# Optimization experiments

Measured on AMD Instinct MI355X. Metric: run time of the kernel, lower is better.

## Reference

```python
import jax, jax.numpy as jnp
import numpy as np

NUM_GROUPS = 32
EPS = 1e-6


def group_norm(x, gamma, beta):
    # x: [B, C, H, W]
    B, C, H, W = x.shape
    xg = x.reshape(B, NUM_GROUPS, C // NUM_GROUPS, H, W)
    mean = jnp.mean(xg, axis=(2, 3, 4), keepdims=True)
    var = jnp.var(xg, axis=(2, 3, 4), keepdims=True)
    xn = (xg - mean) * jax.lax.rsqrt(var + EPS)
    xn = xn.reshape(B, C, H, W)
    return xn * gamma[None, :, None, None] + beta[None, :, None, None]


def conv1x1(x, w, b):
    # x: [B, C, H, W], w: [Cout, Cin], b: [Cout]
    return jnp.einsum('bchw,dc->bdhw', x, w) + b[None, :, None, None]


def setup_inputs() -> dict:
    key = jax.random.key(0)
    ks = jax.random.split(key, 11)
    B, C, H, W = 4, 512, 64, 64
    s = 1.0 / np.sqrt(C)
    return {
        'x': jax.random.normal(ks[0], (B, C, H, W), dtype=jnp.float32),
        'gn_gamma': jnp.ones((C,), dtype=jnp.float32),
        'gn_beta': jnp.zeros((C,), dtype=jnp.float32),
        'wq': jax.random.normal(ks[1], (C, C), dtype=jnp.float32) * s,
        'bq': jax.random.normal(ks[2], (C,), dtype=jnp.float32) * 0.01,
        'wk': jax.random.normal(ks[3], (C, C), dtype=jnp.float32) * s,
        'bk': jax.random.normal(ks[4], (C,), dtype=jnp.float32) * 0.01,
        'wv': jax.random.normal(ks[5], (C, C), dtype=jnp.float32) * s,
        'bv': jax.random.normal(ks[6], (C,), dtype=jnp.float32) * 0.01,
        'wo': jax.random.normal(ks[7], (C, C), dtype=jnp.float32) * s,
        'bo': jax.random.normal(ks[8], (C,), dtype=jnp.float32) * 0.01,
    }


def reference(x, gn_gamma, gn_beta, wq, bq, wk, bk, wv, bv, wo, bo):
    B, C, H, W = x.shape
    h = group_norm(x, gn_gamma, gn_beta)
    q = conv1x1(h, wq, bq).reshape(B, C, H * W)  # [B, C, N]
    k = conv1x1(h, wk, bk).reshape(B, C, H * W)
    v = conv1x1(h, wv, bv).reshape(B, C, H * W)
    scale = jnp.asarray(C, x.dtype) ** -0.5
    # scores[b, i, j] = q_i . k_j
    scores = jnp.einsum('bci,bcj->bij', q, k) * scale  # [B, N, N]
    attn = jax.nn.softmax(scores, axis=2)
    # out[b, c, i] = sum_j v[b, c, j] * attn[b, i, j]
    out = jnp.einsum('bcj,bij->bci', v, attn).reshape(B, C, H, W)
    out = conv1x1(out, wo, bo)
    return x + out
```

## Files before the change

kernel.cpp:

```cpp
#include <hip/hip_runtime.h>

using uint = unsigned int;
typedef short bf16x8 __attribute__((ext_vector_type(8)));
typedef _Float16 f16x8 __attribute__((ext_vector_type(8)));
typedef float f32x4 __attribute__((ext_vector_type(4)));
typedef long i64;
typedef i64 i64x2 __attribute__((ext_vector_type(2)));

static constexpr int Cc = 512;
static constexpr int Nn = 4096;
static constexpr size_t NC = (size_t)Nn * Cc;
static constexpr size_t SN = (size_t)Nn * Nn;

__device__ __forceinline__ unsigned short f2bf(float f) {
    unsigned int u = __builtin_bit_cast(unsigned int, f);
    u = (u + 0x7fff + ((u >> 16) & 1)) >> 16;
    return (unsigned short)u;
}
__device__ __forceinline__ unsigned short f2h(float f) {
    _Float16 h = (_Float16)f;
    return __builtin_bit_cast(unsigned short, h);
}
__device__ __forceinline__ int perm64(int k) {
    return (k & ~63) | ((k & 0x18) << 1) | ((k & 0x20) >> 2) | (k & 7);
}

__device__ __forceinline__ void gll16(const void* g, void* l) {
    __builtin_amdgcn_global_load_lds(
        (const __attribute__((address_space(1))) void*)g,
        (__attribute__((address_space(3))) void*)l, 16, 0, 0);
}

__global__ void cvt_kernel(const float* __restrict__ in, unsigned short* __restrict__ out, int n4) {
    int i = blockIdx.x * blockDim.x + threadIdx.x;
    if (i < n4) {
        float4 v = ((const float4*)in)[i];
        out[i * 4 + 0] = f2bf(v.x);
        out[i * 4 + 1] = f2bf(v.y);
        out[i * 4 + 2] = f2bf(v.z);
        out[i * 4 + 3] = f2bf(v.w);
    }
}

__global__ void zero_kernel(float* __restrict__ p, int n4) {
    int i = blockIdx.x * blockDim.x + threadIdx.x;
    if (i < n4) ((float4*)p)[i] = make_float4(0.f, 0.f, 0.f, 0.f);
}

__global__ void gn_stats_kernel(const float* __restrict__ x, float* __restrict__ meanb,
                                float* __restrict__ rsb) {
    int bg = blockIdx.x;
    const float* slab = x + (size_t)bg * 16 * Nn;
    const float4* s4 = (const float4*)slab;
    int t = threadIdx.x;
    float s1 = 0.f, s2 = 0.f;
#pragma unroll 8
    for (int k = 0; k < 64; ++k) {
        float4 v = s4[k * 256 + t];
        s1 += v.x + v.y + v.z + v.w;
        s2 += v.x * v.x + v.y * v.y + v.z * v.z + v.w * v.w;
    }
#pragma unroll
    for (int o = 32; o > 0; o >>= 1) { s1 += __shfl_down(s1, o); s2 += __shfl_down(s2, o); }
    __shared__ float r1[4], r2[4];
    int wv_ = t >> 6, ln = t & 63;
    if (ln == 0) { r1[wv_] = s1; r2[wv_] = s2; }
    __syncthreads();
    if (t == 0) {
        float a1 = r1[0] + r1[1] + r1[2] + r1[3];
        float a2 = r2[0] + r2[1] + r2[2] + r2[3];
        float mean = a1 * (1.f / 65536.f);
        float var = a2 * (1.f / 65536.f) - mean * mean;
        meanb[bg] = mean;
        rsb[bg] = rsqrtf(var + 1e-6f);
    }
}

__global__ __launch_bounds__(256) void gn_norm_kernel(
    const float* __restrict__ x, const float* __restrict__ meanb, const float* __restrict__ rsb,
    const float* __restrict__ gamma, const float* __restrict__ beta,
    unsigned short* __restrict__ h_t) {
    __shared__ float tile[64][65];
    int n0 = blockIdx.x * 64, c0 = blockIdx.y * 64, b = blockIdx.z;
    int t = threadIdx.x;
    const float* xb = x + (size_t)b * Cc * Nn;
#pragma unroll
    for (int j = 0; j < 4; ++j) {
        int i = j * 256 + t;
        int c = i >> 4;
        int n4 = i & 15;
        int cg = c0 + c;
        float4 v = ((const float4*)(xb + (size_t)cg * Nn + n0))[n4];
        int g = cg >> 4;
        float mean = meanb[b * 32 + g], rs = rsb[b * 32 + g];
        float ga = gamma[cg] * rs;
        float be = beta[cg] - mean * ga;
        tile[n4 * 4 + 0][c] = v.x * ga + be;
        tile[n4 * 4 + 1][c] = v.y * ga + be;
        tile[n4 * 4 + 2][c] = v.z * ga + be;
        tile[n4 * 4 + 3][c] = v.w * ga + be;
    }
    __syncthreads();
    int n = t >> 2;
    int cpart = (t & 3) * 16;
    unsigned short o[16];
#pragma unroll
    for (int q = 0; q < 16; ++q) o[q] = f2bf(tile[n][cpart + q]);
    unsigned short* dst = h_t + (size_t)b * NC + (size_t)(n0 + n) * Cc + c0 + cpart;
    ((uint4*)dst)[0] = ((uint4*)o)[0];
    ((uint4*)dst)[1] = ((uint4*)o)[1];
}

template <int BM, int DT, int BIAS_MODE, int OUT_MODE, int HAS_RES>
__global__ __launch_bounds__(256, 2) void gemm_bt(
    const unsigned short* __restrict__ A, int lda, size_t sA,
    const unsigned short* __restrict__ Bt, int ldb, size_t sB,
    void* __restrict__ outp, int ldc, size_t sC,
    const float* __restrict__ bias,
    const float* __restrict__ res, size_t sR,
    int K, float alpha) {
    constexpr int MT = BM / 32;
    __shared__ unsigned short lA[2][BM * 64];
    __shared__ unsigned short lB[2][128 * 64];
    int z = blockIdx.z;
    A += (size_t)z * sA;
    Bt += (size_t)z * sB;
    int m0 = blockIdx.y * BM, n0 = blockIdx.x * 128;
    int t = threadIdx.x;
    int lane = t & 63, wave = t >> 6;
    int wm = wave >> 1, wn = wave & 1;
    int lo = lane & 15, quad = lane >> 4;

    f32x4 acc[MT][4];
#pragma unroll
    for (int a1 = 0; a1 < MT; ++a1)
#pragma unroll
        for (int a2 = 0; a2 < 4; ++a2) acc[a1][a2] = (f32x4){0.f, 0.f, 0.f, 0.f};

    auto stage = [&](int buf, int k0) {
#pragma unroll
        for (int p = 0; p < MT; ++p) {
            int ci = p * 256 + t;
            int row = ci >> 3;
            int gs = (ci ^ row) & 7;
            gll16(A + (size_t)(m0 + row) * lda + k0 + gs * 8, &lA[buf][ci * 8]);
        }
#pragma unroll
        for (int p = 0; p < 4; ++p) {
            int ci = p * 256 + t;
            int row = ci >> 3;
            int gs = (ci ^ row) & 7;
            gll16(Bt + (size_t)(n0 + row) * ldb + k0 + gs * 8, &lB[buf][ci * 8]);
        }
    };

    int nk = K >> 6;
    stage(0, 0);
    __syncthreads();
    int cur = 0;
    for (int it = 0; it < nk; ++it) {
        if (it + 1 < nk) stage(cur ^ 1, (it + 1) << 6);
#pragma unroll
        for (int ks = 0; ks < 2; ++ks) {
            int G = quad + ks * 4;
            bf16x8 af[MT], bfr[4];
#pragma unroll
            for (int mt = 0; mt < MT; ++mt) {
                int R = wm * (BM / 2) + mt * 16 + lo;
                af[mt] = *(const bf16x8*)&lA[cur][R * 64 + (((G ^ R) & 7) << 3)];
            }
#pragma unroll
            for (int nt = 0; nt < 4; ++nt) {
                int R = wn * 64 + nt * 16 + lo;
                bfr[nt] = *(const bf16x8*)&lB[cur][R * 64 + (((G ^ R) & 7) << 3)];
            }
#pragma unroll
            for (int mt = 0; mt < MT; ++mt)
#pragma unroll
                for (int nt = 0; nt < 4; ++nt) {
                    if (DT == 0)
                        acc[mt][nt] = __builtin_amdgcn_mfma_f32_16x16x32_bf16(af[mt], bfr[nt], acc[mt][nt], 0, 0, 0);
                    else
                        acc[mt][nt] = __builtin_amdgcn_mfma_f32_16x16x32_f16(
                            __builtin_bit_cast(f16x8, af[mt]), __builtin_bit_cast(f16x8, bfr[nt]),
                            acc[mt][nt], 0, 0, 0);
                }
        }
        __syncthreads();
        cur ^= 1;
    }

    size_t zc = (size_t)z * sC;
    float* outf = (float*)outp + zc;
    unsigned short* outb = (unsigned short*)outp + zc;
    unsigned char* outc = (unsigned char*)outp + zc;
    const float* resz = HAS_RES ? res + (size_t)z * sR : nullptr;

#pragma unroll
    for (int mt = 0; mt < MT; ++mt) {
#pragma unroll
        for (int nt = 0; nt < 4; ++nt) {
            int row = m0 + wm * (BM / 2) + mt * 16 + quad * 4;
            int col = n0 + wn * 64 + nt * 16 + lo;
            float bn = (BIAS_MODE == 2) ? bias[col] : 0.f;
#pragma unroll
            for (int r = 0; r < 4; ++r) {
                float vv = acc[mt][nt][r];
                if (BIAS_MODE == 1) vv += bias[row + r];
                if (BIAS_MODE == 2) vv += bn;
                vv *= alpha;
                if (OUT_MODE == 3) {
                    float e = fmaxf(fminf(vv, 448.f), -448.f);
                    int pk = __builtin_amdgcn_cvt_pk_fp8_f32(e, e, 0, false);
                    outc[(size_t)(row + r) * ldc + perm64(col)] = (unsigned char)(pk & 0xff);
                } else {
                    size_t off = (size_t)(row + r) * ldc + col;
                    if (HAS_RES) vv += resz[off];
                    if (OUT_MODE == 0) outf[off] = vv;
                    else if (OUT_MODE == 1) outb[off] = f2bf(vv);
                    else outb[off] = f2h(vv);
                }
            }
        }
    }
}


__global__ __launch_bounds__(256, 2) void qk_fp8(
    const unsigned char* __restrict__ Q, const unsigned char* __restrict__ Kt,
    unsigned char* __restrict__ S, float* __restrict__ lsum, float alpha) {
    __shared__ unsigned char lA[3][256 * 64];
    __shared__ unsigned char lB[3][128 * 64];
    int z = blockIdx.z;
    Q += (size_t)z * NC;
    Kt += (size_t)z * NC;
    S += (size_t)z * SN;
    lsum += (size_t)z * Nn;
    int m0 = blockIdx.y * 256, n0 = blockIdx.x * 128;
    int t = threadIdx.x;
    int lane = t & 63, wave = t >> 6;
    int wm = wave >> 1, wn = wave & 1;
    int lo = lane & 15, quad = lane >> 4;

    f32x4 acc[8][4];
#pragma unroll
    for (int a1 = 0; a1 < 8; ++a1)
#pragma unroll
        for (int a2 = 0; a2 < 4; ++a2) acc[a1][a2] = (f32x4){0.f, 0.f, 0.f, 0.f};

    auto stage = [&](int buf, int it) {
        int k0 = it * 64;
#pragma unroll
        for (int p = 0; p < 4; ++p) {
            int ci = p * 256 + t;
            int line = ci >> 3;
            int slot = (ci & 7) ^ (line & 7);
            int row = (line << 1) | (slot >> 2);
            int g = slot & 3;
            gll16(Q + (size_t)(m0 + row) * Cc + k0 + g * 16, &lA[buf][ci * 16]);
        }
#pragma unroll
        for (int p = 0; p < 2; ++p) {
            int ci = p * 256 + t;
            int line = ci >> 3;
            int slot = (ci & 7) ^ (line & 7);
            int row = (line << 1) | (slot >> 2);
            int g = slot & 3;
            gll16(Kt + (size_t)(n0 + row) * Cc + k0 + g * 16, &lB[buf][ci * 16]);
        }
    };

    stage(0, 0);
    __builtin_amdgcn_sched_barrier(0);
    stage(1, 1);
    __builtin_amdgcn_sched_barrier(0);
    for (int it = 0; it < 8; ++it) {
        asm volatile("s_waitcnt vmcnt(6)" ::: "memory");
        __builtin_amdgcn_s_barrier();
        asm volatile("" ::: "memory");
        __builtin_amdgcn_sched_barrier(0);
        if (it + 2 < 8) stage((it + 2) % 3, it + 2);
        __builtin_amdgcn_sched_barrier(0);
        int cur = it % 3;
        i64x2 aq[8], bq[4];
#pragma unroll
        for (int mt = 0; mt < 8; ++mt) {
            int R = wm * 128 + mt * 16 + lo;
            int line = R >> 1;
            int slot = (((R & 1) << 2) | quad) ^ (line & 7);
            aq[mt] = *(const i64x2*)&lA[cur][line * 128 + slot * 16];
        }
#pragma unroll
        for (int nt = 0; nt < 4; ++nt) {
            int R = wn * 64 + nt * 16 + lo;
            int line = R >> 1;
            int slot = (((R & 1) << 2) | quad) ^ (line & 7);
            bq[nt] = *(const i64x2*)&lB[cur][line * 128 + slot * 16];
        }
#pragma unroll
        for (int ks = 0; ks < 2; ++ks)
#pragma unroll
            for (int mt = 0; mt < 8; ++mt)
#pragma unroll
                for (int nt = 0; nt < 4; ++nt)
                    acc[mt][nt] = __builtin_amdgcn_mfma_f32_16x16x32_fp8_fp8(
                        aq[mt][ks], bq[nt][ks], acc[mt][nt], 0, 0, 0);
    }

#pragma unroll
    for (int mt = 0; mt < 8; ++mt) {
        int row = m0 + wm * 128 + mt * 16 + quad * 4;
        float rsum[4] = {0.f, 0.f, 0.f, 0.f};
#pragma unroll
        for (int nt = 0; nt < 4; ++nt) {
            int col = n0 + wn * 64 + nt * 16 + lo;
            int colp = perm64(col);
#pragma unroll
            for (int r = 0; r < 4; ++r) {
                float e = __expf(acc[mt][nt][r] * alpha - 2.f);
                e = fminf(e, 448.f);
                int pk = __builtin_amdgcn_cvt_pk_fp8_f32(e, e, 0, false);
                S[(size_t)(row + r) * Nn + colp] = (unsigned char)(pk & 0xff);
                rsum[r] += __builtin_amdgcn_cvt_f32_fp8(pk, 0);
            }
        }
#pragma unroll
        for (int o = 1; o < 16; o <<= 1) {
#pragma unroll
            for (int r = 0; r < 4; ++r) rsum[r] += __shfl_xor(rsum[r], o);
        }
        if (lo == 0) {
#pragma unroll
            for (int r = 0; r < 4; ++r) atomicAdd(&lsum[row + r], rsum[r]);
        }
    }
}

__global__ __launch_bounds__(256, 3) void pv_fp8(
    const unsigned char* __restrict__ S, const unsigned char* __restrict__ V,
    const float* __restrict__ lsum, unsigned short* __restrict__ o_t) {
    __shared__ unsigned char lA[3][128 * 64];
    __shared__ unsigned char lB[3][128 * 64];
    int z = blockIdx.z;
    S += (size_t)z * SN;
    V += (size_t)z * NC;
    lsum += (size_t)z * Nn;
    o_t += (size_t)z * NC;
    int m0 = blockIdx.y * 128, n0 = blockIdx.x * 128;
    int t = threadIdx.x;
    int lane = t & 63, wave = t >> 6;
    int wm = wave >> 1, wn = wave & 1;
    int lo = lane & 15, quad = lane >> 4;

    f32x4 acc[4][4];
#pragma unroll
    for (int a1 = 0; a1 < 4; ++a1)
#pragma unroll
        for (int a2 = 0; a2 < 4; ++a2) acc[a1][a2] = (f32x4){0.f, 0.f, 0.f, 0.f};

    auto stage = [&](int buf, int it) {
        int k0 = it * 64;
#pragma unroll
        for (int p = 0; p < 2; ++p) {
            int ci = p * 256 + t;
            int line = ci >> 3;
            int slot = (ci & 7) ^ (line & 7);
            int row = (line << 1) | (slot >> 2);
            int g = slot & 3;
            gll16(S + (size_t)(m0 + row) * Nn + k0 + g * 16, &lA[buf][ci * 16]);
        }
#pragma unroll
        for (int p = 0; p < 2; ++p) {
            int ci = p * 256 + t;
            int line = ci >> 3;
            int slot = (ci & 7) ^ (line & 7);
            int row = (line << 1) | (slot >> 2);
            int g = slot & 3;
            gll16(V + (size_t)(n0 + row) * Nn + k0 + g * 16, &lB[buf][ci * 16]);
        }
    };

    stage(0, 0);
    __builtin_amdgcn_sched_barrier(0);
    stage(1, 1);
    __builtin_amdgcn_sched_barrier(0);
    for (int it = 0; it < 64; ++it) {
        asm volatile("s_waitcnt vmcnt(4)" ::: "memory");
        __builtin_amdgcn_s_barrier();
        asm volatile("" ::: "memory");
        __builtin_amdgcn_sched_barrier(0);
        if (it + 2 < 64) stage((it + 2) % 3, it + 2);
        __builtin_amdgcn_sched_barrier(0);
        int cur = it % 3;
        i64x2 aq[4], bq[4];
#pragma unroll
        for (int mt = 0; mt < 4; ++mt) {
            int R = wm * 64 + mt * 16 + lo;
            int line = R >> 1;
            int slot = (((R & 1) << 2) | quad) ^ (line & 7);
            aq[mt] = *(const i64x2*)&lA[cur][line * 128 + slot * 16];
        }
#pragma unroll
        for (int nt = 0; nt < 4; ++nt) {
            int R = wn * 64 + nt * 16 + lo;
            int line = R >> 1;
            int slot = (((R & 1) << 2) | quad) ^ (line & 7);
            bq[nt] = *(const i64x2*)&lB[cur][line * 128 + slot * 16];
        }
#pragma unroll
        for (int ks = 0; ks < 2; ++ks)
#pragma unroll
            for (int mt = 0; mt < 4; ++mt)
#pragma unroll
                for (int nt = 0; nt < 4; ++nt)
                    acc[mt][nt] = __builtin_amdgcn_mfma_f32_16x16x32_fp8_fp8(
                        aq[mt][ks], bq[nt][ks], acc[mt][nt], 0, 0, 0);
    }

#pragma unroll
    for (int mt = 0; mt < 4; ++mt)
#pragma unroll
        for (int nt = 0; nt < 4; ++nt) {
            int row = m0 + wm * 64 + mt * 16 + quad * 4;
            int col = n0 + wn * 64 + nt * 16 + lo;
#pragma unroll
            for (int r = 0; r < 4; ++r) {
                float vv = acc[mt][nt][r] / lsum[row + r];
                o_t[(size_t)(row + r) * Cc + col] = f2bf(vv);
            }
        }
}

extern "C" void kernel_launch(void* const* d_in, const int* in_sizes, int n_in,
                              void* d_out, int out_size, void* d_ws, size_t ws_size,
                              hipStream_t stream) {
    const float* x     = (const float*)d_in[0];
    const float* gamma = (const float*)d_in[1];
    const float* beta  = (const float*)d_in[2];
    const float* wq = (const float*)d_in[3];
    const float* bq = (const float*)d_in[4];
    const float* wk = (const float*)d_in[5];
    const float* bk = (const float*)d_in[6];
    const float* wv = (const float*)d_in[7];
    const float* bv = (const float*)d_in[8];
    const float* wo = (const float*)d_in[9];
    const float* bo = (const float*)d_in[10];

    char* ws = (char*)d_ws;
    unsigned short* h_t  = (unsigned short*)(ws);
    unsigned char*  q_8  = (unsigned char*)(ws + 16777216);
    unsigned char*  k_8  = (unsigned char*)(ws + 33554432);
    unsigned char*  v_8  = (unsigned char*)(ws + 50331648);
    unsigned short* o_t  = (unsigned short*)(ws + 67108864);
    unsigned char*  S    = (unsigned char*)(ws + 83886080);
    unsigned short* wqb  = (unsigned short*)(ws + 218103808);
    unsigned short* wkb  = (unsigned short*)(ws + 218628096);
    unsigned short* wvb  = (unsigned short*)(ws + 219152384);
    unsigned short* wob  = (unsigned short*)(ws + 219676672);
    float* statm         = (float*)(ws + 220200960);
    float* statr         = (float*)(ws + 220201984);
    float* lsum          = (float*)(ws + 220203008);

    const float SCALE = 0.044194173824159216f;

    cvt_kernel<<<256, 256, 0, stream>>>(wq, wqb, 65536);
    cvt_kernel<<<256, 256, 0, stream>>>(wk, wkb, 65536);
    cvt_kernel<<<256, 256, 0, stream>>>(wv, wvb, 65536);
    cvt_kernel<<<256, 256, 0, stream>>>(wo, wob, 65536);
    zero_kernel<<<16, 256, 0, stream>>>(lsum, 4096);

    gn_stats_kernel<<<128, 256, 0, stream>>>(x, statm, statr);
    gn_norm_kernel<<<dim3(64, 8, 4), 256, 0, stream>>>(x, statm, statr, gamma, beta, h_t);

    gemm_bt<128, 0, 2, 3, 0><<<dim3(4, 32, 4), 256, 0, stream>>>(
        h_t, Cc, NC, wqb, Cc, 0, q_8, Cc, NC, bq, nullptr, 0, Cc, 1.f);
    gemm_bt<128, 0, 2, 3, 0><<<dim3(4, 32, 4), 256, 0, stream>>>(
        h_t, Cc, NC, wkb, Cc, 0, k_8, Cc, NC, bk, nullptr, 0, Cc, 1.f);
    gemm_bt<128, 0, 1, 3, 0><<<dim3(32, 4, 4), 256, 0, stream>>>(
        wvb, Cc, 0, h_t, Cc, NC, v_8, Nn, NC, bv, nullptr, 0, Cc, 1.f);

    qk_fp8<<<dim3(32, 16, 4), 256, 0, stream>>>(q_8, k_8, S, lsum, SCALE);
    pv_fp8<<<dim3(4, 32, 4), 256, 0, stream>>>(S, v_8, lsum, o_t);

    gemm_bt<128, 0, 1, 0, 1><<<dim3(32, 4, 4), 256, 0, stream>>>(
        wob, Cc, 0, o_t, Cc, NC, d_out, Nn, NC, bo, x, NC, Cc, 1.f);
}
```

Before: 327.1 us.

## Use per-wave private LDS staging without block barriers in attention GEMMs

The QK and PV fp8 kernels now have each wave load its own 64x64 A and B slices into a private double-buffered LDS region. This removes the block-wide s_barrier per K step, and MFMA issue is raised in priority with s_setprio. QK tiles shrink from 256x128 to 128x128 and the grid doubles. Separately, the bf16 projection GEMM loses its double buffering and now loads synchronously with two barriers per step. In exchange, neighbouring waves no longer share loads, so global traffic is duplicated (each A/B slice is fetched twice), and projection GEMM latency is exposed.

```diff
diff --git a/kernel.cpp b/kernel.cpp
--- a/kernel.cpp
+++ b/kernel.cpp
@@ -120,8 +120,8 @@
     const float* __restrict__ res, size_t sR,
     int K, float alpha) {
     constexpr int MT = BM / 32;
-    __shared__ unsigned short lA[2][BM * 64];
-    __shared__ unsigned short lB[2][128 * 64];
+    __shared__ unsigned short lA[BM * 64];
+    __shared__ unsigned short lB[128 * 64];
     int z = blockIdx.z;
     A += (size_t)z * sA;
     Bt += (size_t)z * sB;
@@ -137,29 +137,22 @@
 #pragma unroll
         for (int a2 = 0; a2 < 4; ++a2) acc[a1][a2] = (f32x4){0.f, 0.f, 0.f, 0.f};
 
-    auto stage = [&](int buf, int k0) {
+    for (int k0 = 0; k0 < K; k0 += 64) {
 #pragma unroll
         for (int p = 0; p < MT; ++p) {
             int ci = p * 256 + t;
             int row = ci >> 3;
             int gs = (ci ^ row) & 7;
-            gll16(A + (size_t)(m0 + row) * lda + k0 + gs * 8, &lA[buf][ci * 8]);
+            gll16(A + (size_t)(m0 + row) * lda + k0 + gs * 8, &lA[(size_t)ci * 8]);
         }
 #pragma unroll
         for (int p = 0; p < 4; ++p) {
             int ci = p * 256 + t;
             int row = ci >> 3;
             int gs = (ci ^ row) & 7;
-            gll16(Bt + (size_t)(n0 + row) * ldb + k0 + gs * 8, &lB[buf][ci * 8]);
-        }
-    };
-
-    int nk = K >> 6;
-    stage(0, 0);
-    __syncthreads();
-    int cur = 0;
-    for (int it = 0; it < nk; ++it) {
-        if (it + 1 < nk) stage(cur ^ 1, (it + 1) << 6);
+            gll16(Bt + (size_t)(n0 + row) * ldb + k0 + gs * 8, &lB[(size_t)ci * 8]);
+        }
+        __syncthreads();
 #pragma unroll
         for (int ks = 0; ks < 2; ++ks) {
             int G = quad + ks * 4;
@@ -167,12 +160,12 @@
 #pragma unroll
             for (int mt = 0; mt < MT; ++mt) {
                 int R = wm * (BM / 2) + mt * 16 + lo;
-                af[mt] = *(const bf16x8*)&lA[cur][R * 64 + (((G ^ R) & 7) << 3)];
+                af[mt] = *(const bf16x8*)&lA[R * 64 + (((G ^ R) & 7) << 3)];
             }
 #pragma unroll
             for (int nt = 0; nt < 4; ++nt) {
                 int R = wn * 64 + nt * 16 + lo;
-                bfr[nt] = *(const bf16x8*)&lB[cur][R * 64 + (((G ^ R) & 7) << 3)];
+                bfr[nt] = *(const bf16x8*)&lB[R * 64 + (((G ^ R) & 7) << 3)];
             }
 #pragma unroll
             for (int mt = 0; mt < MT; ++mt)
@@ -187,7 +180,6 @@
                 }
         }
         __syncthreads();
-        cur ^= 1;
     }
 
     size_t zc = (size_t)z * sC;
@@ -229,22 +221,23 @@
 __global__ __launch_bounds__(256, 2) void qk_fp8(
     const unsigned char* __restrict__ Q, const unsigned char* __restrict__ Kt,
     unsigned char* __restrict__ S, float* __restrict__ lsum, float alpha) {
-    __shared__ unsigned char lA[3][256 * 64];
-    __shared__ unsigned char lB[3][128 * 64];
+    __shared__ unsigned char lds[4][2][2][4096];
     int z = blockIdx.z;
     Q += (size_t)z * NC;
     Kt += (size_t)z * NC;
     S += (size_t)z * SN;
     lsum += (size_t)z * Nn;
-    int m0 = blockIdx.y * 256, n0 = blockIdx.x * 128;
+    int m0 = blockIdx.y * 128, n0 = blockIdx.x * 128;
     int t = threadIdx.x;
     int lane = t & 63, wave = t >> 6;
     int wm = wave >> 1, wn = wave & 1;
     int lo = lane & 15, quad = lane >> 4;
-
-    f32x4 acc[8][4];
-#pragma unroll
-    for (int a1 = 0; a1 < 8; ++a1)
+    const unsigned char* Arow = Q + (size_t)(m0 + wm * 64) * Cc;
+    const unsigned char* Brow = Kt + (size_t)(n0 + wn * 64) * Cc;
+
+    f32x4 acc[4][4];
+#pragma unroll
+    for (int a1 = 0; a1 < 4; ++a1)
 #pragma unroll
         for (int a2 = 0; a2 < 4; ++a2) acc[a1][a2] = (f32x4){0.f, 0.f, 0.f, 0.f};
 
@@ -252,64 +245,71 @@
         int k0 = it * 64;
 #pragma unroll
         for (int p = 0; p < 4; ++p) {
-            int ci = p * 256 + t;
+            int ci = p * 64 + lane;
             int line = ci >> 3;
             int slot = (ci & 7) ^ (line & 7);
             int row = (line << 1) | (slot >> 2);
             int g = slot & 3;
-            gll16(Q + (size_t)(m0 + row) * Cc + k0 + g * 16, &lA[buf][ci * 16]);
-        }
-#pragma unroll
-        for (int p = 0; p < 2; ++p) {
-            int ci = p * 256 + t;
+            gll16(Arow + (size_t)row * Cc + k0 + g * 16, &lds[wave][buf][0][ci * 16]);
+        }
+#pragma unroll
+        for (int p = 0; p < 4; ++p) {
+            int ci = p * 64 + lane;
             int line = ci >> 3;
             int slot = (ci & 7) ^ (line & 7);
             int row = (line << 1) | (slot >> 2);
             int g = slot & 3;
-            gll16(Kt + (size_t)(n0 + row) * Cc + k0 + g * 16, &lB[buf][ci * 16]);
+            gll16(Brow + (size_t)row * Cc + k0 + g * 16, &lds[wave][buf][1][ci * 16]);
         }
     };
 
-    stage(0, 0);
-    __builtin_amdgcn_sched_barrier(0);
-    stage(1, 1);
-    __builtin_amdgcn_sched_barrier(0);
-    for (int it = 0; it < 8; ++it) {
-        asm volatile("s_waitcnt vmcnt(6)" ::: "memory");
-        __builtin_amdgcn_s_barrier();
-        asm volatile("" ::: "memory");
-        __builtin_amdgcn_sched_barrier(0);
-        if (it + 2 < 8) stage((it + 2) % 3, it + 2);
-        __builtin_amdgcn_sched_barrier(0);
-        int cur = it % 3;
-        i64x2 aq[8], bq[4];
-#pragma unroll
-        for (int mt = 0; mt < 8; ++mt) {
-            int R = wm * 128 + mt * 16 + lo;
+    auto compute = [&](int buf, bool dost, int sit) {
+        const unsigned char* A = &lds[wave][buf][0][0];
+        const unsigned char* B = &lds[wave][buf][1][0];
+        i64x2 aq[4], bq[4];
+#pragma unroll
+        for (int mt = 0; mt < 4; ++mt) {
+            int R = mt * 16 + lo;
             int line = R >> 1;
             int slot = (((R & 1) << 2) | quad) ^ (line & 7);
-            aq[mt] = *(const i64x2*)&lA[cur][line * 128 + slot * 16];
+            aq[mt] = *(const i64x2*)&A[line * 128 + slot * 16];
         }
 #pragma unroll
         for (int nt = 0; nt < 4; ++nt) {
-            int R = wn * 64 + nt * 16 + lo;
+            int R = nt * 16 + lo;
             int line = R >> 1;
             int slot = (((R & 1) << 2) | quad) ^ (line & 7);
-            bq[nt] = *(const i64x2*)&lB[cur][line * 128 + slot * 16];
-        }
+            bq[nt] = *(const i64x2*)&B[line * 128 + slot * 16];
+        }
+        asm volatile("s_waitcnt lgkmcnt(0)" ::: "memory");
+        __builtin_amdgcn_sched_barrier(0);
+        if (dost) stage(buf, sit);
+        __builtin_amdgcn_sched_barrier(0);
+        __builtin_amdgcn_s_setprio(1);
 #pragma unroll
         for (int ks = 0; ks < 2; ++ks)
 #pragma unroll
-            for (int mt = 0; mt < 8; ++mt)
+            for (int mt = 0; mt < 4; ++mt)
 #pragma unroll
                 for (int nt = 0; nt < 4; ++nt)
                     acc[mt][nt] = __builtin_amdgcn_mfma_f32_16x16x32_fp8_fp8(
                         aq[mt][ks], bq[nt][ks], acc[mt][nt], 0, 0, 0);
-    }
-
-#pragma unroll
-    for (int mt = 0; mt < 8; ++mt) {
-        int row = m0 + wm * 128 + mt * 16 + quad * 4;
+        __builtin_amdgcn_s_setprio(0);
+    };
+
+    stage(0, 0);
+    stage(1, 1);
+    for (int it = 0; it < 6; ++it) {
+        asm volatile("s_waitcnt vmcnt(8)" ::: "memory");
+        compute(it & 1, true, it + 2);
+    }
+    asm volatile("s_waitcnt vmcnt(0)" ::: "memory");
+    compute(0, false, 0);
+    compute(1, false, 0);
+
+#pragma unroll
+    for (int mt = 0; mt < 4; ++mt) {
+        int row = m0 + wm * 64 + mt * 16 + quad * 4;
         float rsum[4] = {0.f, 0.f, 0.f, 0.f};
 #pragma unroll
         for (int nt = 0; nt < 4; ++nt) {
@@ -336,11 +336,10 @@
     }
 }
 
-__global__ __launch_bounds__(256, 3) void pv_fp8(
+__global__ __launch_bounds__(256, 2) void pv_fp8(
     const unsigned char* __restrict__ S, const unsigned char* __restrict__ V,
     const float* __restrict__ lsum, unsigned short* __restrict__ o_t) {
-    __shared__ unsigned char lA[3][128 * 64];
-    __shared__ unsigned char lB[3][128 * 64];
+    __shared__ unsigned char lds[4][2][2][4096];
     int z = blockIdx.z;
     S += (size_t)z * SN;
     V += (size_t)z * NC;
@@ -351,6 +350,8 @@
     int lane = t & 63, wave = t >> 6;
     int wm = wave >> 1, wn = wave & 1;
     int lo = lane & 15, quad = lane >> 4;
+    const unsigned char* Arow = S + (size_t)(m0 + wm * 64) * Nn;
+    const unsigned char* Brow = V + (size_t)(n0 + wn * 64) * Nn;
 
     f32x4 acc[4][4];
 #pragma unroll
@@ -361,52 +362,48 @@
     auto stage = [&](int buf, int it) {
         int k0 = it * 64;
 #pragma unroll
-        for (int p = 0; p < 2; ++p) {
-            int ci = p * 256 + t;
+        for (int p = 0; p < 4; ++p) {
+            int ci = p * 64 + lane;
             int line = ci >> 3;
             int slot = (ci & 7) ^ (line & 7);
             int row = (line << 1) | (slot >> 2);
             int g = slot & 3;
-            gll16(S + (size_t)(m0 + row) * Nn + k0 + g * 16, &lA[buf][ci * 16]);
-        }
-#pragma unroll
-        for (int p = 0; p < 2; ++p) {
-            int ci = p * 256 + t;
+            gll16(Arow + (size_t)row * Nn + k0 + g * 16, &lds[wave][buf][0][ci * 16]);
+        }
+#pragma unroll
+        for (int p = 0; p < 4; ++p) {
+            int ci = p * 64 + lane;
             int line = ci >> 3;
             int slot = (ci & 7) ^ (line & 7);
             int row = (line << 1) | (slot >> 2);
             int g = slot & 3;
-            gll16(V + (size_t)(n0 + row) * Nn + k0 + g * 16, &lB[buf][ci * 16]);
+            gll16(Brow + (size_t)row * Nn + k0 + g * 16, &lds[wave][buf][1][ci * 16]);
         }
     };
 
-    stage(0, 0);
-    __builtin_amdgcn_sched_barrier(0);
-    stage(1, 1);
-    __builtin_amdgcn_sched_barrier(0);
-    for (int it = 0; it < 64; ++it) {
-        asm volatile("s_waitcnt vmcnt(4)" ::: "memory");
-        __builtin_amdgcn_s_barrier();
-        asm volatile("" ::: "memory");
-        __builtin_amdgcn_sched_barrier(0);
-        if (it + 2 < 64) stage((it + 2) % 3, it + 2);
-        __builtin_amdgcn_sched_barrier(0);
-        int cur = it % 3;
+    auto compute = [&](int buf, bool dost, int sit) {
+        const unsigned char* A = &lds[wave][buf][0][0];
+        const unsigned char* B = &lds[wave][buf][1][0];
         i64x2 aq[4], bq[4];
 #pragma unroll
         for (int mt = 0; mt < 4; ++mt) {
-            int R = wm * 64 + mt * 16 + lo;
+            int R = mt * 16 + lo;
             int line = R >> 1;
             int slot = (((R & 1) << 2) | quad) ^ (line & 7);
-            aq[mt] = *(const i64x2*)&lA[cur][line * 128 + slot * 16];
+            aq[mt] = *(const i64x2*)&A[line * 128 + slot * 16];
         }
 #pragma unroll
         for (int nt = 0; nt < 4; ++nt) {
-            int R = wn * 64 + nt * 16 + lo;
+            int R = nt * 16 + lo;
             int line = R >> 1;
             int slot = (((R & 1) << 2) | quad) ^ (line & 7);
-            bq[nt] = *(const i64x2*)&lB[cur][line * 128 + slot * 16];
-        }
+            bq[nt] = *(const i64x2*)&B[line * 128 + slot * 16];
+        }
+        asm volatile("s_waitcnt lgkmcnt(0)" ::: "memory");
+        __builtin_amdgcn_sched_barrier(0);
+        if (dost) stage(buf, sit);
+        __builtin_amdgcn_sched_barrier(0);
+        __builtin_amdgcn_s_setprio(1);
 #pragma unroll
         for (int ks = 0; ks < 2; ++ks)
 #pragma unroll
@@ -415,7 +412,18 @@
                 for (int nt = 0; nt < 4; ++nt)
                     acc[mt][nt] = __builtin_amdgcn_mfma_f32_16x16x32_fp8_fp8(
                         aq[mt][ks], bq[nt][ks], acc[mt][nt], 0, 0, 0);
-    }
+        __builtin_amdgcn_s_setprio(0);
+    };
+
+    stage(0, 0);
+    stage(1, 1);
+    for (int it = 0; it < 62; ++it) {
+        asm volatile("s_waitcnt vmcnt(8)" ::: "memory");
+        compute(it & 1, true, it + 2);
+    }
+    asm volatile("s_waitcnt vmcnt(0)" ::: "memory");
+    compute(0, false, 0);
+    compute(1, false, 0);
 
 #pragma unroll
     for (int mt = 0; mt < 4; ++mt)
@@ -479,7 +487,7 @@
     gemm_bt<128, 0, 1, 3, 0><<<dim3(32, 4, 4), 256, 0, stream>>>(
         wvb, Cc, 0, h_t, Cc, NC, v_8, Nn, NC, bv, nullptr, 0, Cc, 1.f);
 
-    qk_fp8<<<dim3(32, 16, 4), 256, 0, stream>>>(q_8, k_8, S, lsum, SCALE);
+    qk_fp8<<<dim3(32, 32, 4), 256, 0, stream>>>(q_8, k_8, S, lsum, SCALE);
     pv_fp8<<<dim3(4, 32, 4), 256, 0, stream>>>(S, v_8, lsum, o_t);
 
     gemm_bt<128, 0, 1, 0, 1><<<dim3(32, 4, 4), 256, 0, stream>>>(
```

Result: slower. 344.1 us (+5.2%).
